# Performance work log

Hardware: AMD Instinct MI355X
Metric: run time of the kernel (lower is better)

## Reference

```python
import jax, jax.numpy as jnp
import numpy as np

B, S, H, NH = 8, 1024, 768, 12
DK = H // NH  # 64


def setup_inputs() -> dict:
    key = jax.random.key(0)
    ks = jax.random.split(key, 7)
    sc = 0.02
    return {
        "Q": jax.random.normal(ks[0], (B, S, H), jnp.float32),
        "K": jax.random.normal(ks[1], (B, S, H), jnp.float32),
        "V": jax.random.normal(ks[2], (B, S, H), jnp.float32),
        "Wq": jax.random.normal(ks[3], (H, H), jnp.float32) * sc,
        "Wk": jax.random.normal(ks[4], (H, H), jnp.float32) * sc,
        "Wv": jax.random.normal(ks[5], (H, H), jnp.float32) * sc,
        "Wo": jax.random.normal(ks[6], (H, H), jnp.float32) * sc,
    }


def reference(Q, K, V, Wq, Wk, Wv, Wo):
    # torch Linear(bias=False): y = x @ W.T, weight shape [out, in]
    q = jnp.einsum('bsh,oh->bso', Q, Wq).reshape(B, S, NH, DK)
    k = jnp.einsum('bsh,oh->bso', K, Wk).reshape(B, S, NH, DK)
    v = jnp.einsum('bsh,oh->bso', V, Wv).reshape(B, S, NH, DK)
    # naive SDPA per head: full [B,NH,S,S] score matrix, scale by sqrt(dk)
    scores = jnp.einsum('bqnd,bknd->bnqk', q, k) / jnp.sqrt(jnp.float32(DK))
    w = jax.nn.softmax(scores, axis=-1)
    c = jnp.einsum('bnqk,bknd->bqnd', w, v).reshape(B, S, H)
    return jnp.einsum('bsh,oh->bso', c, Wo)
```

## Files before the change

### kernel.cpp

```cpp
#include <hip/hip_runtime.h>
#include <hip/hip_bf16.h>

#define B_   8
#define S_   1024
#define H_   768
#define NH_  12
#define DK_  64
#define M_   (B_ * S_)

typedef __attribute__((ext_vector_type(8))) short          short8;
typedef __attribute__((ext_vector_type(8))) unsigned short ushort8;
typedef __attribute__((ext_vector_type(4))) unsigned short ushort4v;
typedef __attribute__((ext_vector_type(4))) float          f32x4;

__device__ __forceinline__ unsigned short f2bf(float x) {
    union { __hip_bfloat16 h; unsigned short u; } r;
    r.h = __float2bfloat16(x);
    return r.u;
}

__device__ __forceinline__ unsigned cvtpk_bf16(float lo, float hi) {
    unsigned r;
    asm("v_cvt_pk_bf16_f32 %0, %1, %2" : "=v"(r) : "v"(lo), "v"(hi));
    return r;
}

__device__ __forceinline__ void glds16(const unsigned short* g, unsigned short* l) {
    __builtin_amdgcn_global_load_lds(
        (const __attribute__((address_space(1))) unsigned int*)g,
        (__attribute__((address_space(3))) unsigned int*)l, 16, 0, 0);
}

__global__ __launch_bounds__(256)
void cvt_w(const float* __restrict__ w0, const float* __restrict__ w1,
           const float* __restrict__ w2, const float* __restrict__ w3,
           unsigned short* __restrict__ o0, unsigned short* __restrict__ o1,
           unsigned short* __restrict__ o2, unsigned short* __restrict__ o3)
{
    const int wsel = blockIdx.y;
    const float* src = (wsel == 0) ? w0 : (wsel == 1) ? w1 : (wsel == 2) ? w2 : w3;
    unsigned short* dst = (wsel == 0) ? o0 : (wsel == 1) ? o1 : (wsel == 2) ? o2 : o3;
    const float s = (wsel == 0) ? 0.125f * 1.44269504089f : 1.0f;
    const int i = blockIdx.x * 256 + threadIdx.x;
    const float4 x = ((const float4*)src)[i];
    ushort4v o;
    o[0] = f2bf(x.x * s); o[1] = f2bf(x.y * s);
    o[2] = f2bf(x.z * s); o[3] = f2bf(x.w * s);
    ((ushort4v*)dst)[i] = o;
}

template<bool A_BF16, bool OUT_BF16>
__global__ __launch_bounds__(256)
void gemm_bt(const void* __restrict__ A0, const void* __restrict__ A1,
             const void* __restrict__ A2,
             const unsigned short* __restrict__ W0,
             const unsigned short* __restrict__ W1,
             const unsigned short* __restrict__ W2,
             void* __restrict__ C0, void* __restrict__ C1, void* __restrict__ C2)
{
    __shared__ unsigned short As[128 * 32];
    __shared__ unsigned short Bs[128 * 32];

    const int tid  = threadIdx.x;
    const int bid  = blockIdx.x;
    const int x    = bid & 7, j = bid >> 3;
    const int z    = j / 48;
    const int r48  = j % 48;
    const int bm   = x * 8 + r48 / 6;
    const int bn   = r48 % 6;

    const int w    = tid >> 6, lane = tid & 63;
    const int lg   = lane >> 4, lc = lane & 15;
    const int wm   = (w >> 1) * 64, wn = (w & 1) * 64;

    const void* Av = (z == 0) ? A0 : (z == 1) ? A1 : A2;
    const unsigned short* Bw = (z == 0) ? W0 : (z == 1) ? W1 : W2;
    void* Cv = (z == 0) ? C0 : (z == 1) ? C1 : C2;

    const float*          Af = (const float*)Av;
    const unsigned short* Ah = (const unsigned short*)Av;

    const int srow = tid >> 2;
    const int sc8  = (tid & 3) * 8;

    const unsigned short* gB  = &Bw[(size_t)(bn * 128 + srow) * H_ + sc8];
    unsigned short* ldsB0 = &Bs[w * 512];
    unsigned short* ldsB1 = &Bs[2048 + w * 512];

    const unsigned short* gAh = A_BF16 ? &Ah[(size_t)(bm * 128 + srow) * H_ + sc8] : nullptr;
    const float*          gAf = A_BF16 ? nullptr : &Af[(size_t)(bm * 128 + srow) * H_ + sc8];
    unsigned short* ldsA0 = &As[w * 512];
    unsigned short* ldsA1 = &As[2048 + w * 512];

    f32x4 acc[4][4] = {};

    for (int k0 = 0; k0 < H_; k0 += 32) {
        glds16(gB + k0, ldsB0);
        glds16(gB + (size_t)64 * H_ + k0, ldsB1);
        if (A_BF16) {
            glds16(gAh + k0, ldsA0);
            glds16(gAh + (size_t)64 * H_ + k0, ldsA1);
        } else {
#pragma unroll
            for (int i = 0; i < 2; i++) {
                const float4 x0 = *(const float4*)(gAf + (size_t)i * 64 * H_ + k0);
                const float4 x1 = *(const float4*)(gAf + (size_t)i * 64 * H_ + k0 + 4);
                ushort8 o8;
                o8[0] = f2bf(x0.x); o8[1] = f2bf(x0.y);
                o8[2] = f2bf(x0.z); o8[3] = f2bf(x0.w);
                o8[4] = f2bf(x1.x); o8[5] = f2bf(x1.y);
                o8[6] = f2bf(x1.z); o8[7] = f2bf(x1.w);
                *(ushort8*)&As[(i * 64 + srow) * 32 + sc8] = o8;
            }
        }
        __syncthreads();

        short8 af[4], bfr[4];
#pragma unroll
        for (int mi = 0; mi < 4; mi++)
            af[mi] = *(const short8*)&As[(wm + mi * 16 + lc) * 32 + lg * 8];
#pragma unroll
        for (int ni = 0; ni < 4; ni++)
            bfr[ni] = *(const short8*)&Bs[(wn + ni * 16 + lc) * 32 + lg * 8];
#pragma unroll
        for (int mi = 0; mi < 4; mi++)
#pragma unroll
            for (int ni = 0; ni < 4; ni++)
                acc[mi][ni] = __builtin_amdgcn_mfma_f32_16x16x32_bf16(
                    af[mi], bfr[ni], acc[mi][ni], 0, 0, 0);
        __syncthreads();
    }

#pragma unroll
    for (int mi = 0; mi < 4; mi++)
#pragma unroll
        for (int ni = 0; ni < 4; ni++)
#pragma unroll
            for (int reg = 0; reg < 4; reg++) {
                const int row = bm * 128 + wm + mi * 16 + lg * 4 + reg;
                const int col = bn * 128 + wn + ni * 16 + lc;
                if (OUT_BF16)
                    ((unsigned short*)Cv)[(size_t)row * H_ + col] = f2bf(acc[mi][ni][reg]);
                else
                    ((float*)Cv)[(size_t)row * H_ + col] = acc[mi][ni][reg];
            }
}

__global__ __launch_bounds__(256)
void transpose_v(const unsigned short* __restrict__ v,
                 unsigned short* __restrict__ vt)
{
    __shared__ unsigned short T[64][72];
    const int tid = threadIdx.x;
    const int st0 = blockIdx.x, h = blockIdx.y, b = blockIdx.z;
    const int r = tid >> 2, d0 = (tid & 3) * 16, g = tid & 3;

    const unsigned short* src = &v[(size_t)(b * S_ + st0 * 64 + r) * H_ + h * DK_ + d0];
    const ushort8 v0 = *(const ushort8*)src;
    const ushort8 v1 = *(const ushort8*)(src + 8);
    const int colv = r ^ (g << 4);
#pragma unroll
    for (int j = 0; j < 8; j++) T[d0 + j][colv]     = v0[j];
#pragma unroll
    for (int j = 0; j < 8; j++) T[d0 + 8 + j][colv] = v1[j];
    __syncthreads();

    const size_t ob = ((size_t)(b * NH_ + h) * DK_) * S_ + st0 * 64;
#pragma unroll
    for (int half = 0; half < 2; half++) {
        const int ci = half * 256 + tid;
        const int d = ci >> 3, kc = ci & 7;
        const int sw = ((d >> 4) & 3) << 4;
        const ushort8 val = *(const ushort8*)&T[d][(kc * 8) ^ sw];
        *(ushort8*)&vt[ob + (size_t)d * S_ + kc * 8] = val;
    }
}

__global__ __launch_bounds__(256)
void attn(const unsigned short* __restrict__ q,
          const unsigned short* __restrict__ k,
          const unsigned short* __restrict__ vt,
          unsigned short* __restrict__ c)
{
    __shared__ unsigned short Ks[64][72];
    __shared__ unsigned short Vs[64][72];

    const int tid  = threadIdx.x;
    const int qt   = blockIdx.x, h = blockIdx.y, b = blockIdx.z;
    const int wid  = tid >> 6;
    const int lane = tid & 63;
    const int lg   = lane >> 4, lc = lane & 15;
    const int r    = tid >> 2;
    const int g    = tid & 3;
    const int d0   = g * 16;
    const size_t base = (size_t)b * S_ * H_ + (size_t)h * DK_;
    const size_t vtb  = (size_t)(b * NH_ + h) * DK_ * S_;

    short8 aq[2][2];
#pragma unroll
    for (int m = 0; m < 2; m++)
#pragma unroll
        for (int ks = 0; ks < 2; ks++)
            aq[m][ks] = *(const short8*)
                &q[base + (size_t)(qt * 128 + wid * 32 + m * 16 + lc) * H_ + ks * 32 + lg * 8];

    f32x4 o[2][4] = {};
    float lsum[2] = {0.f, 0.f};

    for (int kt = 0; kt < S_ / 64; kt++) {
        {
            const unsigned short* ksrc = &k[base + (size_t)(kt * 64 + r) * H_ + d0];
            *(ushort8*)&Ks[r][d0]     = *(const ushort8*)ksrc;
            *(ushort8*)&Ks[r][d0 + 8] = *(const ushort8*)(ksrc + 8);
            const unsigned short* vsrc = &vt[vtb + (size_t)r * S_ + kt * 64 + d0];
            *(ushort8*)&Vs[r][d0]     = *(const ushort8*)vsrc;
            *(ushort8*)&Vs[r][d0 + 8] = *(const ushort8*)(vsrc + 8);
        }
        __syncthreads();

        f32x4 st[2][4] = {};
        __builtin_amdgcn_s_setprio(1);
#pragma unroll
        for (int ni = 0; ni < 4; ni++)
#pragma unroll
            for (int ks = 0; ks < 2; ks++) {
                const short8 bk = *(const short8*)&Ks[ni * 16 + lc][ks * 32 + lg * 8];
                st[0][ni] = __builtin_amdgcn_mfma_f32_16x16x32_bf16(bk, aq[0][ks], st[0][ni], 0, 0, 0);
                st[1][ni] = __builtin_amdgcn_mfma_f32_16x16x32_bf16(bk, aq[1][ks], st[1][ni], 0, 0, 0);
            }
        __builtin_amdgcn_s_setprio(0);

        unsigned pw[2][4][2];
#pragma unroll
        for (int m = 0; m < 2; m++) {
#pragma unroll
            for (int ni = 0; ni < 4; ni++) {
#pragma unroll
                for (int reg = 0; reg < 4; reg++) {
                    const float pp = exp2f(st[m][ni][reg]);
                    st[m][ni][reg] = pp;
                    lsum[m] += pp;
                }
                pw[m][ni][0] = cvtpk_bf16(st[m][ni][0], st[m][ni][1]);
                pw[m][ni][1] = cvtpk_bf16(st[m][ni][2], st[m][ni][3]);
            }
        }

        const int sl0 = lc + ((lg & 1) << 5);
        const int sl1 = sl0 + 16;
        const bool hi = (lg >> 1) != 0;
        short8 pa[2][2];
#pragma unroll
        for (int m = 0; m < 2; m++)
#pragma unroll
            for (int ks = 0; ks < 2; ks++) {
                const unsigned lo0 = pw[m][2 * ks][0],     lo1 = pw[m][2 * ks][1];
                const unsigned hi0 = pw[m][2 * ks + 1][0], hi1 = pw[m][2 * ks + 1][1];
                union { unsigned u[4]; short8 s8; } pk;
                const unsigned a0l = __shfl(lo0, sl0, 64), a0h = __shfl(hi0, sl0, 64);
                const unsigned a1l = __shfl(lo1, sl0, 64), a1h = __shfl(hi1, sl0, 64);
                const unsigned a2l = __shfl(lo0, sl1, 64), a2h = __shfl(hi0, sl1, 64);
                const unsigned a3l = __shfl(lo1, sl1, 64), a3h = __shfl(hi1, sl1, 64);
                pk.u[0] = hi ? a0h : a0l;
                pk.u[1] = hi ? a1h : a1l;
                pk.u[2] = hi ? a2h : a2l;
                pk.u[3] = hi ? a3h : a3l;
                pa[m][ks] = pk.s8;
            }

        __builtin_amdgcn_s_setprio(1);
#pragma unroll
        for (int ni = 0; ni < 4; ni++)
#pragma unroll
            for (int ks = 0; ks < 2; ks++) {
                const short8 bv = *(const short8*)&Vs[ni * 16 + lc][ks * 32 + lg * 8];
                o[0][ni] = __builtin_amdgcn_mfma_f32_16x16x32_bf16(pa[0][ks], bv, o[0][ni], 0, 0, 0);
                o[1][ni] = __builtin_amdgcn_mfma_f32_16x16x32_bf16(pa[1][ks], bv, o[1][ni], 0, 0, 0);
            }
        __builtin_amdgcn_s_setprio(0);
        __syncthreads();
    }

#pragma unroll
    for (int m = 0; m < 2; m++) {
        float l = lsum[m];
        l += __shfl_xor(l, 16, 64);
        l += __shfl_xor(l, 32, 64);
        const float iv = 1.0f / l;
#pragma unroll
        for (int reg = 0; reg < 4; reg++) {
            const float ivr = __shfl(iv, lg * 4 + reg, 64);
            const int row = qt * 128 + wid * 32 + m * 16 + lg * 4 + reg;
#pragma unroll
            for (int ni = 0; ni < 4; ni++)
                c[base + (size_t)row * H_ + ni * 16 + lc] = f2bf(o[m][ni][reg] * ivr);
        }
    }
}

extern "C" void kernel_launch(void* const* d_in, const int* in_sizes, int n_in,
                              void* d_out, int out_size, void* d_ws, size_t ws_size,
                              hipStream_t stream)
{
    const float* Q  = (const float*)d_in[0];
    const float* K  = (const float*)d_in[1];
    const float* V  = (const float*)d_in[2];
    const float* Wq = (const float*)d_in[3];
    const float* Wk = (const float*)d_in[4];
    const float* Wv = (const float*)d_in[5];
    const float* Wo = (const float*)d_in[6];

    unsigned short* qb = (unsigned short*)d_ws;
    unsigned short* kb = qb + (size_t)M_ * H_;
    unsigned short* vb = kb + (size_t)M_ * H_;
    unsigned short* vtb = vb + (size_t)M_ * H_;
    unsigned short* cb  = vb;
    unsigned short* wq = vtb + (size_t)M_ * H_;
    unsigned short* wk = wq + (size_t)H_ * H_;
    unsigned short* wv = wk + (size_t)H_ * H_;
    unsigned short* wo = wv + (size_t)H_ * H_;

    cvt_w<<<dim3(H_ * H_ / 4 / 256, 4), 256, 0, stream>>>(
        Wq, Wk, Wv, Wo, wq, wk, wv, wo);

    gemm_bt<false, true><<<dim3(64 * 6 * 3), 256, 0, stream>>>(
        Q, K, V, wq, wk, wv, qb, kb, vb);

    transpose_v<<<dim3(S_ / 64, NH_, B_), 256, 0, stream>>>(vb, vtb);

    attn<<<dim3(S_ / 128, NH_, B_), 256, 0, stream>>>(qb, kb, vtb, cb);

    gemm_bt<true, false><<<dim3(64 * 6), 256, 0, stream>>>(
        cb, cb, cb, wo, wo, wo, d_out, d_out, d_out);
}
```

Baseline: 157.7 us.

## Double-buffer LDS tiles in projection GEMM to overlap loads with MFMA

Converts the projection GEMM main loop to a double-buffered LDS pipeline. The next k-tile is prefetched via direct-to-LDS loads, or for fp32 inputs converted in registers and stored after the MFMAs, while the current tile is multiplied. One barrier per iteration is removed. It also raises wave priority around the MFMA block and adds an occupancy hint to launch bounds. In exchange it doubles shared memory and adds register pressure.

Result: slower. 162.5 us (+3.1%).

```diff
diff --git a/kernel.cpp b/kernel.cpp
--- a/kernel.cpp
+++ b/kernel.cpp
@@ -50,7 +50,7 @@
 }
 
 template<bool A_BF16, bool OUT_BF16>
-__global__ __launch_bounds__(256)
+__global__ __launch_bounds__(256, 4)
 void gemm_bt(const void* __restrict__ A0, const void* __restrict__ A1,
              const void* __restrict__ A2,
              const unsigned short* __restrict__ W0,
@@ -58,8 +58,8 @@
              const unsigned short* __restrict__ W2,
              void* __restrict__ C0, void* __restrict__ C1, void* __restrict__ C2)
 {
-    __shared__ unsigned short As[128 * 32];
-    __shared__ unsigned short Bs[128 * 32];
+    __shared__ unsigned short As[2][128 * 32];
+    __shared__ unsigned short Bs[2][128 * 32];
 
     const int tid  = threadIdx.x;
     const int bid  = blockIdx.x;
@@ -84,51 +84,83 @@
     const int sc8  = (tid & 3) * 8;
 
     const unsigned short* gB  = &Bw[(size_t)(bn * 128 + srow) * H_ + sc8];
-    unsigned short* ldsB0 = &Bs[w * 512];
-    unsigned short* ldsB1 = &Bs[2048 + w * 512];
-
     const unsigned short* gAh = A_BF16 ? &Ah[(size_t)(bm * 128 + srow) * H_ + sc8] : nullptr;
     const float*          gAf = A_BF16 ? nullptr : &Af[(size_t)(bm * 128 + srow) * H_ + sc8];
-    unsigned short* ldsA0 = &As[w * 512];
-    unsigned short* ldsA1 = &As[2048 + w * 512];
-
+
+    const int NK = H_ / 32;
     f32x4 acc[4][4] = {};
-
-    for (int k0 = 0; k0 < H_; k0 += 32) {
-        glds16(gB + k0, ldsB0);
-        glds16(gB + (size_t)64 * H_ + k0, ldsB1);
-        if (A_BF16) {
-            glds16(gAh + k0, ldsA0);
-            glds16(gAh + (size_t)64 * H_ + k0, ldsA1);
-        } else {
-#pragma unroll
-            for (int i = 0; i < 2; i++) {
-                const float4 x0 = *(const float4*)(gAf + (size_t)i * 64 * H_ + k0);
-                const float4 x1 = *(const float4*)(gAf + (size_t)i * 64 * H_ + k0 + 4);
-                ushort8 o8;
-                o8[0] = f2bf(x0.x); o8[1] = f2bf(x0.y);
-                o8[2] = f2bf(x0.z); o8[3] = f2bf(x0.w);
-                o8[4] = f2bf(x1.x); o8[5] = f2bf(x1.y);
-                o8[6] = f2bf(x1.z); o8[7] = f2bf(x1.w);
-                *(ushort8*)&As[(i * 64 + srow) * 32 + sc8] = o8;
-            }
-        }
-        __syncthreads();
+    ushort8 a8[2];
+
+    glds16(gB, &Bs[0][w * 512]);
+    glds16(gB + (size_t)64 * H_, &Bs[0][2048 + w * 512]);
+    if (A_BF16) {
+        glds16(gAh, &As[0][w * 512]);
+        glds16(gAh + (size_t)64 * H_, &As[0][2048 + w * 512]);
+    } else {
+#pragma unroll
+        for (int i = 0; i < 2; i++) {
+            const float4 x0 = *(const float4*)(gAf + (size_t)i * 64 * H_);
+            const float4 x1 = *(const float4*)(gAf + (size_t)i * 64 * H_ + 4);
+            ushort8 o8;
+            o8[0] = f2bf(x0.x); o8[1] = f2bf(x0.y);
+            o8[2] = f2bf(x0.z); o8[3] = f2bf(x0.w);
+            o8[4] = f2bf(x1.x); o8[5] = f2bf(x1.y);
+            o8[6] = f2bf(x1.z); o8[7] = f2bf(x1.w);
+            *(ushort8*)&As[0][(i * 64 + srow) * 32 + sc8] = o8;
+        }
+    }
+    __syncthreads();
+
+    int buf = 0;
+    for (int t = 0; t < NK; t++) {
+        const bool more = (t + 1 < NK);
+        const int  k0n  = (t + 1) * 32;
+        const int  nb   = buf ^ 1;
+
+        if (more) {
+            glds16(gB + k0n, &Bs[nb][w * 512]);
+            glds16(gB + (size_t)64 * H_ + k0n, &Bs[nb][2048 + w * 512]);
+            if (A_BF16) {
+                glds16(gAh + k0n, &As[nb][w * 512]);
+                glds16(gAh + (size_t)64 * H_ + k0n, &As[nb][2048 + w * 512]);
+            } else {
+#pragma unroll
+                for (int i = 0; i < 2; i++) {
+                    const float4 x0 = *(const float4*)(gAf + (size_t)i * 64 * H_ + k0n);
+                    const float4 x1 = *(const float4*)(gAf + (size_t)i * 64 * H_ + k0n + 4);
+                    ushort8 o8;
+                    o8[0] = f2bf(x0.x); o8[1] = f2bf(x0.y);
+                    o8[2] = f2bf(x0.z); o8[3] = f2bf(x0.w);
+                    o8[4] = f2bf(x1.x); o8[5] = f2bf(x1.y);
+                    o8[6] = f2bf(x1.z); o8[7] = f2bf(x1.w);
+                    a8[i] = o8;
+                }
+            }
+        }
 
         short8 af[4], bfr[4];
 #pragma unroll
         for (int mi = 0; mi < 4; mi++)
-            af[mi] = *(const short8*)&As[(wm + mi * 16 + lc) * 32 + lg * 8];
+            af[mi] = *(const short8*)&As[buf][(wm + mi * 16 + lc) * 32 + lg * 8];
 #pragma unroll
         for (int ni = 0; ni < 4; ni++)
-            bfr[ni] = *(const short8*)&Bs[(wn + ni * 16 + lc) * 32 + lg * 8];
+            bfr[ni] = *(const short8*)&Bs[buf][(wn + ni * 16 + lc) * 32 + lg * 8];
+        __builtin_amdgcn_s_setprio(1);
 #pragma unroll
         for (int mi = 0; mi < 4; mi++)
 #pragma unroll
             for (int ni = 0; ni < 4; ni++)
                 acc[mi][ni] = __builtin_amdgcn_mfma_f32_16x16x32_bf16(
                     af[mi], bfr[ni], acc[mi][ni], 0, 0, 0);
+        __builtin_amdgcn_s_setprio(0);
+
+        if (more && !A_BF16) {
+#pragma unroll
+            for (int i = 0; i < 2; i++)
+                *(ushort8*)&As[nb][(i * 64 + srow) * 32 + sc8] = a8[i];
+        }
         __syncthreads();
+        buf = nb;
     }
 
 #pragma unroll
```

## Double GEMM K-tile to 64 with XOR-swizzled LDS layout and MFMA priority

Applied to the files above, without the earlier changes.

The projection GEMM's K step grows from 32 to 64, which halves the number of barrier pairs per tile. The LDS tiles switch to a 64-wide row layout with an XOR swizzle on 16-byte chunks, applied both to the global-to-LDS loads and to the fp32-converted A stores, to avoid bank conflicts on fragment reads. MFMA blocks are wrapped in s_setprio so compute is favoured over other waves' loads. The cost is double the LDS per block (32 KB), which may reduce occupancy, and more complex address math.

After: 185.1 us. +17.4%, slower.

```diff
diff --git a/kernel.cpp b/kernel.cpp
--- a/kernel.cpp
+++ b/kernel.cpp
@@ -58,8 +58,8 @@
              const unsigned short* __restrict__ W2,
              void* __restrict__ C0, void* __restrict__ C1, void* __restrict__ C2)
 {
-    __shared__ unsigned short As[128 * 32];
-    __shared__ unsigned short Bs[128 * 32];
+    __shared__ unsigned short As[128 * 64];
+    __shared__ unsigned short Bs[128 * 64];
 
     const int tid  = threadIdx.x;
     const int bid  = blockIdx.x;
@@ -80,54 +80,62 @@
     const float*          Af = (const float*)Av;
     const unsigned short* Ah = (const unsigned short*)Av;
 
-    const int srow = tid >> 2;
-    const int sc8  = (tid & 3) * 8;
-
-    const unsigned short* gB  = &Bw[(size_t)(bn * 128 + srow) * H_ + sc8];
-    unsigned short* ldsB0 = &Bs[w * 512];
-    unsigned short* ldsB1 = &Bs[2048 + w * 512];
-
-    const unsigned short* gAh = A_BF16 ? &Ah[(size_t)(bm * 128 + srow) * H_ + sc8] : nullptr;
-    const float*          gAf = A_BF16 ? nullptr : &Af[(size_t)(bm * 128 + srow) * H_ + sc8];
-    unsigned short* ldsA0 = &As[w * 512];
-    unsigned short* ldsA1 = &As[2048 + w * 512];
+    const int srow8 = lane >> 3;
+    const int scb   = (lane & 7) ^ srow8;
+    const unsigned short* gB0 = &Bw[(size_t)(bn * 128 + w * 32 + srow8) * H_ + scb * 8];
+    const unsigned short* gA0 = A_BF16 ?
+        &Ah[(size_t)(bm * 128 + w * 32 + srow8) * H_ + scb * 8] : nullptr;
+
+    const int arow  = tid >> 1;
+    const int ahalf = tid & 1;
+    const float* gAf = A_BF16 ? nullptr :
+        &Af[(size_t)(bm * 128 + arow) * H_ + ahalf * 32];
 
     f32x4 acc[4][4] = {};
 
-    for (int k0 = 0; k0 < H_; k0 += 32) {
-        glds16(gB + k0, ldsB0);
-        glds16(gB + (size_t)64 * H_ + k0, ldsB1);
-        if (A_BF16) {
-            glds16(gAh + k0, ldsA0);
-            glds16(gAh + (size_t)64 * H_ + k0, ldsA1);
-        } else {
-#pragma unroll
-            for (int i = 0; i < 2; i++) {
-                const float4 x0 = *(const float4*)(gAf + (size_t)i * 64 * H_ + k0);
-                const float4 x1 = *(const float4*)(gAf + (size_t)i * 64 * H_ + k0 + 4);
+    for (int t = 0; t < H_ / 64; t++) {
+        const int k0 = t * 64;
+
+#pragma unroll
+        for (int i = 0; i < 4; i++) {
+            glds16(gB0 + (size_t)i * 8 * H_ + k0, &Bs[(w * 4 + i) * 512]);
+            if (A_BF16)
+                glds16(gA0 + (size_t)i * 8 * H_ + k0, &As[(w * 4 + i) * 512]);
+        }
+        if (!A_BF16) {
+#pragma unroll
+            for (int jj = 0; jj < 4; jj++) {
+                const float4 x0 = *(const float4*)(gAf + k0 + jj * 8);
+                const float4 x1 = *(const float4*)(gAf + k0 + jj * 8 + 4);
                 ushort8 o8;
                 o8[0] = f2bf(x0.x); o8[1] = f2bf(x0.y);
                 o8[2] = f2bf(x0.z); o8[3] = f2bf(x0.w);
                 o8[4] = f2bf(x1.x); o8[5] = f2bf(x1.y);
                 o8[6] = f2bf(x1.z); o8[7] = f2bf(x1.w);
-                *(ushort8*)&As[(i * 64 + srow) * 32 + sc8] = o8;
+                *(ushort8*)&As[arow * 64 + (((ahalf * 4 + jj) ^ (arow & 7)) * 8)] = o8;
             }
         }
         __syncthreads();
 
-        short8 af[4], bfr[4];
-#pragma unroll
-        for (int mi = 0; mi < 4; mi++)
-            af[mi] = *(const short8*)&As[(wm + mi * 16 + lc) * 32 + lg * 8];
-#pragma unroll
-        for (int ni = 0; ni < 4; ni++)
-            bfr[ni] = *(const short8*)&Bs[(wn + ni * 16 + lc) * 32 + lg * 8];
-#pragma unroll
-        for (int mi = 0; mi < 4; mi++)
+#pragma unroll
+        for (int kk = 0; kk < 2; kk++) {
+            const int cbl = ((kk * 4 + lg) ^ (lc & 7)) * 8;
+            short8 af[4], bfr[4];
+#pragma unroll
+            for (int mi = 0; mi < 4; mi++)
+                af[mi] = *(const short8*)&As[(wm + mi * 16 + lc) * 64 + cbl];
 #pragma unroll
             for (int ni = 0; ni < 4; ni++)
-                acc[mi][ni] = __builtin_amdgcn_mfma_f32_16x16x32_bf16(
-                    af[mi], bfr[ni], acc[mi][ni], 0, 0, 0);
+                bfr[ni] = *(const short8*)&Bs[(wn + ni * 16 + lc) * 64 + cbl];
+            __builtin_amdgcn_s_setprio(1);
+#pragma unroll
+            for (int mi = 0; mi < 4; mi++)
+#pragma unroll
+                for (int ni = 0; ni < 4; ni++)
+                    acc[mi][ni] = __builtin_amdgcn_mfma_f32_16x16x32_bf16(
+                        af[mi], bfr[ni], acc[mi][ni], 0, 0, 0);
+            __builtin_amdgcn_s_setprio(0);
+        }
         __syncthreads();
     }
 
```

## Double-buffer LDS tiles in projection GEMM to overlap loads with MFMA

Applied to the files above, without the earlier changes.

The projection GEMM now uses two LDS buffers per operand and issues the global loads (and fp32-to-bf16 conversion of A) for the next k-tile before running the MFMAs on the current tile. This halves the number of barriers per k-step and is meant to hide global-load latency behind compute. It also raises wave priority around the MFMA block with s_setprio. The cost is double the LDS footprint, which may reduce occupancy, and more live registers for the staged A values.

After: 153.5 us. 2.7% less time.

```diff
diff --git a/kernel.cpp b/kernel.cpp
--- a/kernel.cpp
+++ b/kernel.cpp
@@ -49,6 +49,54 @@
     ((ushort4v*)dst)[i] = o;
 }
 
+#define GEMM_ISSUE(AsX, BsX, k0)                                              \
+  {                                                                           \
+    glds16(gB + (k0), (BsX) + w * 512);                                       \
+    glds16(gB + (size_t)64 * H_ + (k0), (BsX) + 2048 + w * 512);              \
+    if (A_BF16) {                                                             \
+      glds16(gAh + (k0), (AsX) + w * 512);                                    \
+      glds16(gAh + (size_t)64 * H_ + (k0), (AsX) + 2048 + w * 512);           \
+    } else {                                                                  \
+      _Pragma("unroll")                                                       \
+      for (int i = 0; i < 2; i++) {                                           \
+        const float4 x0 = *(const float4*)(gAf + (size_t)i * 64 * H_ + (k0));  \
+        const float4 x1 = *(const float4*)(gAf + (size_t)i * 64 * H_ + (k0) + 4);\
+        ushort8 o8;                                                           \
+        o8[0] = f2bf(x0.x); o8[1] = f2bf(x0.y);                               \
+        o8[2] = f2bf(x0.z); o8[3] = f2bf(x0.w);                               \
+        o8[4] = f2bf(x1.x); o8[5] = f2bf(x1.y);                               \
+        o8[6] = f2bf(x1.z); o8[7] = f2bf(x1.w);                               \
+        a8[i] = o8;                                                           \
+      }                                                                       \
+    }                                                                         \
+  }
+
+#define GEMM_WRITE_A(AsX)                                                     \
+  if (!A_BF16) {                                                              \
+    _Pragma("unroll")                                                         \
+    for (int i = 0; i < 2; i++)                                               \
+      *(ushort8*)&(AsX)[(i * 64 + srow) * 32 + sc8] = a8[i];                  \
+  }
+
+#define GEMM_COMPUTE(AsX, BsX)                                                \
+  {                                                                           \
+    short8 af[4], bfr[4];                                                     \
+    _Pragma("unroll")                                                         \
+    for (int mi = 0; mi < 4; mi++)                                            \
+      af[mi] = *(const short8*)&(AsX)[(wm + mi * 16 + lc) * 32 + lg * 8];     \
+    _Pragma("unroll")                                                         \
+    for (int ni = 0; ni < 4; ni++)                                            \
+      bfr[ni] = *(const short8*)&(BsX)[(wn + ni * 16 + lc) * 32 + lg * 8];    \
+    __builtin_amdgcn_s_setprio(1);                                            \
+    _Pragma("unroll")                                                         \
+    for (int mi = 0; mi < 4; mi++)                                            \
+      _Pragma("unroll")                                                       \
+      for (int ni = 0; ni < 4; ni++)                                          \
+        acc[mi][ni] = __builtin_amdgcn_mfma_f32_16x16x32_bf16(                \
+            af[mi], bfr[ni], acc[mi][ni], 0, 0, 0);                           \
+    __builtin_amdgcn_s_setprio(0);                                            \
+  }
+
 template<bool A_BF16, bool OUT_BF16>
 __global__ __launch_bounds__(256)
 void gemm_bt(const void* __restrict__ A0, const void* __restrict__ A1,
@@ -58,8 +106,10 @@
              const unsigned short* __restrict__ W2,
              void* __restrict__ C0, void* __restrict__ C1, void* __restrict__ C2)
 {
-    __shared__ unsigned short As[128 * 32];
-    __shared__ unsigned short Bs[128 * 32];
+    __shared__ unsigned short As0[128 * 32];
+    __shared__ unsigned short Bs0[128 * 32];
+    __shared__ unsigned short As1[128 * 32];
+    __shared__ unsigned short Bs1[128 * 32];
 
     const int tid  = threadIdx.x;
     const int bid  = blockIdx.x;
@@ -84,52 +134,34 @@
     const int sc8  = (tid & 3) * 8;
 
     const unsigned short* gB  = &Bw[(size_t)(bn * 128 + srow) * H_ + sc8];
-    unsigned short* ldsB0 = &Bs[w * 512];
-    unsigned short* ldsB1 = &Bs[2048 + w * 512];
-
     const unsigned short* gAh = A_BF16 ? &Ah[(size_t)(bm * 128 + srow) * H_ + sc8] : nullptr;
     const float*          gAf = A_BF16 ? nullptr : &Af[(size_t)(bm * 128 + srow) * H_ + sc8];
-    unsigned short* ldsA0 = &As[w * 512];
-    unsigned short* ldsA1 = &As[2048 + w * 512];
 
     f32x4 acc[4][4] = {};
-
-    for (int k0 = 0; k0 < H_; k0 += 32) {
-        glds16(gB + k0, ldsB0);
-        glds16(gB + (size_t)64 * H_ + k0, ldsB1);
-        if (A_BF16) {
-            glds16(gAh + k0, ldsA0);
-            glds16(gAh + (size_t)64 * H_ + k0, ldsA1);
-        } else {
-#pragma unroll
-            for (int i = 0; i < 2; i++) {
-                const float4 x0 = *(const float4*)(gAf + (size_t)i * 64 * H_ + k0);
-                const float4 x1 = *(const float4*)(gAf + (size_t)i * 64 * H_ + k0 + 4);
-                ushort8 o8;
-                o8[0] = f2bf(x0.x); o8[1] = f2bf(x0.y);
-                o8[2] = f2bf(x0.z); o8[3] = f2bf(x0.w);
-                o8[4] = f2bf(x1.x); o8[5] = f2bf(x1.y);
-                o8[6] = f2bf(x1.z); o8[7] = f2bf(x1.w);
-                *(ushort8*)&As[(i * 64 + srow) * 32 + sc8] = o8;
-            }
-        }
+    ushort8 a8[2];
+
+    GEMM_ISSUE(As0, Bs0, 0);
+    GEMM_WRITE_A(As0);
+    __syncthreads();
+
+#pragma unroll 1
+    for (int t = 0; t < 22; t += 2) {
+        GEMM_ISSUE(As1, Bs1, (t + 1) * 32);
+        GEMM_COMPUTE(As0, Bs0);
+        GEMM_WRITE_A(As1);
         __syncthreads();
 
-        short8 af[4], bfr[4];
-#pragma unroll
-        for (int mi = 0; mi < 4; mi++)
-            af[mi] = *(const short8*)&As[(wm + mi * 16 + lc) * 32 + lg * 8];
-#pragma unroll
-        for (int ni = 0; ni < 4; ni++)
-            bfr[ni] = *(const short8*)&Bs[(wn + ni * 16 + lc) * 32 + lg * 8];
-#pragma unroll
-        for (int mi = 0; mi < 4; mi++)
-#pragma unroll
-            for (int ni = 0; ni < 4; ni++)
-                acc[mi][ni] = __builtin_amdgcn_mfma_f32_16x16x32_bf16(
-                    af[mi], bfr[ni], acc[mi][ni], 0, 0, 0);
+        GEMM_ISSUE(As0, Bs0, (t + 2) * 32);
+        GEMM_COMPUTE(As1, Bs1);
+        GEMM_WRITE_A(As0);
         __syncthreads();
     }
+
+    GEMM_ISSUE(As1, Bs1, 23 * 32);
+    GEMM_COMPUTE(As0, Bs0);
+    GEMM_WRITE_A(As1);
+    __syncthreads();
+    GEMM_COMPUTE(As1, Bs1);
 
 #pragma unroll
     for (int mi = 0; mi < 4; mi++)
@@ -160,9 +192,9 @@
     const ushort8 v1 = *(const ushort8*)(src + 8);
     const int colv = r ^ (g << 4);
 #pragma unroll
-    for (int j = 0; j < 8; j++) T[d0 + j][colv]     = v0[j];
-#pragma unroll
-    for (int j = 0; j < 8; j++) T[d0 + 8 + j][colv] = v1[j];
+    for (int jj = 0; jj < 8; jj++) T[d0 + jj][colv]     = v0[jj];
+#pragma unroll
+    for (int jj = 0; jj < 8; jj++) T[d0 + 8 + jj][colv] = v1[jj];
     __syncthreads();
 
     const size_t ob = ((size_t)(b * NH_ + h) * DK_) * S_ + st0 * 64;
```
